# Optimization experiments

Hardware: AMD Instinct MI355X
Metric: run time of the kernel (lower is better)

## Reference

```python
import jax, jax.numpy as jnp
import numpy as np

B, N, C = 2, 2048, 768
H = 12
D = C // H
SCALE = D ** -0.5
EPS = 1e-5
HID = 4 * C


def layer_norm(x, g, b):
    mu = jnp.mean(x, axis=-1, keepdims=True)
    var = jnp.var(x, axis=-1, keepdims=True)
    return (x - mu) * jax.lax.rsqrt(var + EPS) * g + b


def setup_inputs():
    key = jax.random.key(0)
    ks = jax.random.split(key, 12)
    s = C ** -0.5
    x = jax.random.normal(ks[0], (B, N, C), dtype=jnp.float32)
    mask = (jax.random.uniform(ks[1], (B, N, N)) < 0.1).astype(jnp.float32)
    return {
        "x": x,
        "mask": mask,
        "g1": jnp.ones((C,), jnp.float32),
        "b1": jnp.zeros((C,), jnp.float32),
        "Wq": jax.random.normal(ks[2], (C, C), jnp.float32) * s,
        "Wkv": jax.random.normal(ks[3], (2 * C, C), jnp.float32) * s,
        "Wp": jax.random.normal(ks[4], (C, C), jnp.float32) * s,
        "bp": jnp.zeros((C,), jnp.float32),
        "g2": jnp.ones((C,), jnp.float32),
        "b2": jnp.zeros((C,), jnp.float32),
        "W1": jax.random.normal(ks[5], (HID, C), jnp.float32) * s,
        "bf1": jnp.zeros((HID,), jnp.float32),
        "W2": jax.random.normal(ks[6], (C, HID), jnp.float32) * (HID ** -0.5),
        "bf2": jnpmp if False else jnp.zeros((C,), jnp.float32),
    }


def block_fwd(x, mask, g1, b1, Wq, Wkv, Wp, bp, g2, b2, W1, bf1, W2, bf2):
    # --- attention branch (pre-norm) ---
    xn = layer_norm(x, g1, b1)
    q = (xn @ Wq.T).reshape(B, N, H, D).transpose(0, 2, 1, 3)      # bhnd
    kv = (xn @ Wkv.T).reshape(B, N, 2, H, D).transpose(2, 0, 3, 1, 4)
    k, v = kv[0], kv[1]                                             # bhnd
    attn = jnp.einsum('bhnd,bhmd->bhnm', q, k) * SCALE
    attn = attn + (mask * -100000.0)[:, None]                       # additive mask
    attn = jax.nn.softmax(attn, axis=-1)
    o = jnp.einsum('bhnm,bhmd->bhnd', attn, v)
    o = o.transpose(0, 2, 1, 3).reshape(B, N, C)
    o = o @ Wp.T + bp
    x = x + o
    # --- MLP branch (pre-norm) ---
    xn2 = layer_norm(x, g2, b2)
    h = jax.nn.gelu(xn2 @ W1.T + bf1, approximate=False)
    x = x + (h @ W2.T + bf2)
    return x


def reference(x, mask, g1, b1, Wq, Wkv, Wp, bp, g2, b2, W1, bf1, W2, bf2):
    return block_fwd(x, mask, g1, b1, Wq, Wkv, Wp, bp, g2, b2, W1, bf1, W2, bf2)
```

## Files before the change

kernel.cpp:

```cpp
#include <hip/hip_runtime.h>
#include <hip/hip_bf16.h>
#include <cstdint>
#include <cstddef>

#define BB 2
#define NN 2048
#define CC 768
#define HH 12
#define DD 64
#define HID 3072
#define TT (BB*NN)

typedef __attribute__((ext_vector_type(8))) short bf16x8;
typedef __attribute__((ext_vector_type(4))) short bf16x4;
typedef __attribute__((ext_vector_type(4))) float f32x4;
typedef __attribute__((ext_vector_type(4))) float float4v;
typedef __attribute__((ext_vector_type(4))) unsigned short ushort4v;
typedef __attribute__((ext_vector_type(8))) unsigned short ushort8v;

__device__ __forceinline__ unsigned short f2bf(float f) {
    unsigned int u = __float_as_uint(f);
    u += 0x7fffu + ((u >> 16) & 1u);
    return (unsigned short)(u >> 16);
}
__device__ __forceinline__ float bf2f(unsigned short u) {
    return __uint_as_float(((unsigned int)u) << 16);
}
#if __has_builtin(__builtin_amdgcn_exp2f)
#define EXP2F(x) __builtin_amdgcn_exp2f(x)
#else
#define EXP2F(x) exp2f(x)
#endif

__device__ __forceinline__ void gload16(const void* g, void* l) {
    __builtin_amdgcn_global_load_lds((__attribute__((address_space(1))) unsigned int*)g,
                                     (__attribute__((address_space(3))) unsigned int*)l,
                                     16, 0, 0);
}

#define WAITV(N) asm volatile("s_waitcnt vmcnt(" #N ")" ::: "memory")
#define WAITLGKM asm volatile("s_waitcnt lgkmcnt(0)" ::: "memory")

struct PrepArgs {
    const float* x; const float* g1; const float* b1; unsigned short* xn;
    const float* cin[5]; unsigned short* cout[5]; int n4[5];
    const float* mask; unsigned short* mb;
};
__global__ __launch_bounds__(256) void prep_kernel(PrepArgs a) {
    int id = blockIdx.x;
    int tid = threadIdx.x;
    if (id < TT) {
        const float* xr = a.x + (size_t)id * CC;
        float v0 = xr[tid], v1 = xr[tid + 256], v2 = xr[tid + 512];
        float s = v0 + v1 + v2;
        float s2 = v0 * v0 + v1 * v1 + v2 * v2;
#pragma unroll
        for (int off = 1; off < 64; off <<= 1) {
            s  += __shfl_xor(s, off);
            s2 += __shfl_xor(s2, off);
        }
        __shared__ float red[8];
        int wv = tid >> 6, lane = tid & 63;
        if (lane == 0) { red[wv] = s; red[wv + 4] = s2; }
        __syncthreads();
        s  = red[0] + red[1] + red[2] + red[3];
        s2 = red[4] + red[5] + red[6] + red[7];
        float mu   = s * (1.0f / CC);
        float var  = s2 * (1.0f / CC) - mu * mu;
        float rstd = rsqrtf(var + 1e-5f);
        unsigned short* orow = a.xn + (size_t)id * CC;
        orow[tid]       = f2bf((v0 - mu) * rstd * a.g1[tid]       + a.b1[tid]);
        orow[tid + 256] = f2bf((v1 - mu) * rstd * a.g1[tid + 256] + a.b1[tid + 256]);
        orow[tid + 512] = f2bf((v2 - mu) * rstd * a.g1[tid + 512] + a.b1[tid + 512]);
    } else if (id < TT + 1024) {
        int base = (id - TT) * 256 + tid;
        int stride = 1024 * 256;
#pragma unroll
        for (int sseg = 0; sseg < 5; ++sseg) {
            const float4v* ip = (const float4v*)a.cin[sseg];
            ushort4v* op = (ushort4v*)a.cout[sseg];
            for (int i = base; i < a.n4[sseg]; i += stride) {
                float4v v = ip[i];
                ushort4v o;
                o[0] = f2bf(v[0]); o[1] = f2bf(v[1]); o[2] = f2bf(v[2]); o[3] = f2bf(v[3]);
                op[i] = o;
            }
        }
    } else {
        int base = (id - TT - 1024) * 256 + tid;
        int stride = 1024 * 256;
        int n = BB * NN * (NN / 16);
        for (int i = base; i < n; i += stride) {
            const float4v* mp = (const float4v*)(a.mask + (size_t)i * 16);
            unsigned int bits = 0;
#pragma unroll
            for (int q = 0; q < 4; ++q) {
                float4v v = mp[q];
#pragma unroll
                for (int j = 0; j < 4; ++j) bits |= (v[j] > 0.5f) ? (1u << (q * 4 + j)) : 0u;
            }
            a.mb[i] = (unsigned short)bits;
        }
    }
}

__global__ __launch_bounds__(256) void ln_kernel(const float* __restrict__ x,
                                                 const float* __restrict__ g,
                                                 const float* __restrict__ b,
                                                 unsigned short* __restrict__ out) {
    int t = blockIdx.x;
    int tid = threadIdx.x;
    const float* xr = x + (size_t)t * CC;
    float v0 = xr[tid], v1 = xr[tid + 256], v2 = xr[tid + 512];
    float s = v0 + v1 + v2;
    float s2 = v0 * v0 + v1 * v1 + v2 * v2;
#pragma unroll
    for (int off = 1; off < 64; off <<= 1) {
        s  += __shfl_xor(s, off);
        s2 += __shfl_xor(s2, off);
    }
    __shared__ float red[8];
    int wv = tid >> 6, lane = tid & 63;
    if (lane == 0) { red[wv] = s; red[wv + 4] = s2; }
    __syncthreads();
    s  = red[0] + red[1] + red[2] + red[3];
    s2 = red[4] + red[5] + red[6] + red[7];
    float mu   = s * (1.0f / CC);
    float var  = s2 * (1.0f / CC) - mu * mu;
    float rstd = rsqrtf(var + 1e-5f);
    unsigned short* orow = out + (size_t)t * CC;
    orow[tid]       = f2bf((v0 - mu) * rstd * g[tid]       + b[tid]);
    orow[tid + 256] = f2bf((v1 - mu) * rstd * g[tid + 256] + b[tid + 256]);
    orow[tid + 512] = f2bf((v2 - mu) * rstd * g[tid + 512] + b[tid + 512]);
}

template <int EPI, int BM>
__global__ __launch_bounds__(256) void gemm_bt(const unsigned short* __restrict__ A,
                                               const unsigned short* __restrict__ Bw,
                                               const float* __restrict__ bias,
                                               const float* __restrict__ res,
                                               void* __restrict__ out,
                                               int M, int N, int K) {
    constexpr int MI = BM / 32;
    constexpr int NCA = (BM * 4) / 256;
    __shared__ alignas(16) unsigned short As[2][BM * 32];
    __shared__ alignas(16) unsigned short Bs[2][128 * 32];
    int tid = threadIdx.x;
    int lane = tid & 63, wv = tid >> 6;
    int l16 = lane & 15, lg = lane >> 4;
    int bm = blockIdx.x, bn = blockIdx.y;
    int wm = (wv & 1) * (BM / 2), wn = (wv >> 1) * 64;

    const unsigned short* Ab = A + (size_t)bm * BM * K;
    const unsigned short* Bb = Bw + (size_t)bn * 128 * K;

    const unsigned short* aSrc[NCA]; int aDst[NCA];
#pragma unroll
    for (int i = 0; i < NCA; ++i) {
        int c = tid + i * 256;
        int row = c >> 2, p = c & 3;
        int lc = p ^ ((row >> 1) & 3);
        aSrc[i] = Ab + (size_t)row * K + lc * 8;
        aDst[i] = c * 8;
    }
    const unsigned short* bSrc[2]; int bDst[2];
#pragma unroll
    for (int i = 0; i < 2; ++i) {
        int c = tid + i * 256;
        int row = c >> 2, p = c & 3;
        int lc = p ^ ((row >> 1) & 3);
        bSrc[i] = Bb + (size_t)row * K + lc * 8;
        bDst[i] = c * 8;
    }
    int aoff = (wm + l16) * 32 + ((lg ^ (((wm + l16) >> 1) & 3)) * 8);
    int boff = (wn + l16) * 32 + ((lg ^ (((wn + l16) >> 1) & 3)) * 8);

    f32x4 acc[MI][4];
#pragma unroll
    for (int i = 0; i < MI; ++i)
#pragma unroll
        for (int j = 0; j < 4; ++j) acc[i][j] = f32x4{0.f, 0.f, 0.f, 0.f};

    auto STAGE = [&](int s, int k0) {
#pragma unroll
        for (int i = 0; i < NCA; ++i) gload16(aSrc[i] + k0, &As[s][aDst[i]]);
#pragma unroll
        for (int i = 0; i < 2; ++i)   gload16(bSrc[i] + k0, &Bs[s][bDst[i]]);
    };

    STAGE(0, 0);
    int nt = K / 32;
    for (int t = 0; t < nt; ++t) {
        int cur = t & 1;
        if (t + 1 < nt) {
            STAGE(cur ^ 1, (t + 1) * 32);
            if constexpr (NCA + 2 == 4) { WAITV(4); } else { WAITV(3); }
        } else {
            WAITV(0);
        }
        __builtin_amdgcn_s_barrier();
        bf16x8 af[MI], bfr[4];
#pragma unroll
        for (int mi = 0; mi < MI; ++mi) af[mi]  = *(const bf16x8*)&As[cur][aoff + mi * 512];
#pragma unroll
        for (int ni = 0; ni < 4; ++ni)  bfr[ni] = *(const bf16x8*)&Bs[cur][boff + ni * 512];
#pragma unroll
        for (int mi = 0; mi < MI; ++mi)
#pragma unroll
            for (int ni = 0; ni < 4; ++ni)
                acc[mi][ni] = __builtin_amdgcn_mfma_f32_16x16x32_bf16(bfr[ni], af[mi], acc[mi][ni], 0, 0, 0);
        WAITLGKM;
        __builtin_amdgcn_s_barrier();
    }

#pragma unroll
    for (int mi = 0; mi < MI; ++mi) {
        int row = bm * BM + wm + mi * 16 + l16;
#pragma unroll
        for (int ni = 0; ni < 4; ++ni) {
            int col = bn * 128 + wn + ni * 16 + lg * 4;
            size_t idx = (size_t)row * N + col;
            f32x4 v = acc[mi][ni];
            if (EPI == 0) {
                bf16x4 ov;
#pragma unroll
                for (int r2 = 0; r2 < 4; ++r2) ov[r2] = (short)f2bf(v[r2]);
                *(bf16x4*)((unsigned short*)out + idx) = ov;
            } else if (EPI == 1 || EPI == 3) {
                f32x4 bv = *(const f32x4*)&bias[col];
                f32x4 rv = *(const f32x4*)&res[idx];
                f32x4 ov;
#pragma unroll
                for (int r2 = 0; r2 < 4; ++r2) ov[r2] = v[r2] + bv[r2] + rv[r2];
                *(f32x4*)((float*)out + idx) = ov;
            } else {
                f32x4 bv = *(const f32x4*)&bias[col];
                bf16x4 ov;
#pragma unroll
                for (int r2 = 0; r2 < 4; ++r2) {
                    float t2 = v[r2] + bv[r2];
                    t2 = 0.5f * t2 * (1.0f + erff(t2 * 0.70710678118f));
                    ov[r2] = (short)f2bf(t2);
                }
                *(bf16x4*)((unsigned short*)out + idx) = ov;
            }
        }
    }
}

#define KVB 64
#define HNT 16
#define VP 68
__global__ __launch_bounds__(256) void attn_kernel(const unsigned short* __restrict__ qkv,
                                                   const unsigned short* __restrict__ maskb,
                                                   float* __restrict__ Op,
                                                   float* __restrict__ lp) {
    __shared__ alignas(16) unsigned short Ks[2][64 * 64];
    __shared__ alignas(16) unsigned short Vt[2][64 * VP];
    int tid = threadIdx.x;
    int lane = tid & 63, wv = tid >> 6;
    int l16 = lane & 15, lg = lane >> 4;
    int id = blockIdx.x;
    int half = id & 1;
    int rid = id >> 1;
    int xcd = rid & 7, r = rid >> 3;
    int bh = xcd * 3 + (r % 3);
    int qb = r / 3;
    int b = bh / HH, h = bh % HH;
    int qrow = qb * 64 + wv * 16 + l16;
    int kt0 = half * HNT;

    const unsigned short* qp = qkv + ((size_t)(b * NN + qrow)) * 2304 + h * DD;
    bf16x8 q0r = *(const bf16x8*)(qp + 8 * lg);
    bf16x8 q1r = *(const bf16x8*)(qp + 32 + 8 * lg);
    const float QSC = 0.125f * 1.4426950408889634f;
    bf16x8 q0, q1;
#pragma unroll
    for (int j = 0; j < 8; ++j) {
        q0[j] = (short)f2bf(bf2f((unsigned short)q0r[j]) * QSC);
        q1[j] = (short)f2bf(bf2f((unsigned short)q1r[j]) * QSC);
    }

    const unsigned short* mrow  = maskb + ((size_t)(b * NN + qrow)) * 128;
    const unsigned short* kbase = qkv + (size_t)b * NN * 2304 + 768 + h * DD;
    const unsigned short* vbase = qkv + (size_t)b * NN * 2304 + 1536 + h * DD;

    const unsigned short* kSrc[2]; int kDst[2];
#pragma unroll
    for (int i = 0; i < 2; ++i) {
        int c = tid + i * 256;
        int row = c >> 3, p = c & 7;
        int lc = p ^ (row & 7);
        kSrc[i] = kbase + (size_t)row * 2304 + lc * 8;
        kDst[i] = c * 8;
    }
    int kp = tid & 31, dg = tid >> 5;
    const unsigned short* vSrc = vbase + (size_t)(2 * kp) * 2304 + dg * 8;

    int sw = l16 & 7;
    int kb0 = l16 * 64 + ((lg ^ sw) * 8);
    int kb1 = l16 * 64 + (((lg + 4) ^ sw) * 8);
    int vbo = l16 * VP + lg * 4;

    bf16x8 va, vb;
    unsigned long long mb_cur, mb_nxt;

    f32x4 oa[4];
#pragma unroll
    for (int i = 0; i < 4; ++i) oa[i] = f32x4{0.f, 0.f, 0.f, 0.f};
    float lrun = 0.f;

    auto LOAD = [&](int t, int s) {
        const unsigned short* vp = vSrc + (size_t)t * KVB * 2304;
        va = *(const bf16x8*)(vp);
        vb = *(const bf16x8*)(vp + 2304);
        mb_nxt = *(const unsigned long long*)(mrow + t * 4);
        __builtin_amdgcn_sched_barrier(0);
#pragma unroll
        for (int i = 0; i < 2; ++i) gload16(kSrc[i] + (size_t)t * KVB * 2304, &Ks[s][kDst[i]]);
    };
    auto WRITEV = [&](int s) {
        unsigned int* VtU = (unsigned int*)Vt[s];
#pragma unroll
        for (int j = 0; j < 8; ++j)
            VtU[(dg * 8 + j) * (VP / 2) + kp] =
                (unsigned int)(unsigned short)va[j] | ((unsigned int)(unsigned short)vb[j] << 16);
    };

    LOAD(kt0, 0);
    WAITV(2);
    WRITEV(0);
    mb_cur = mb_nxt;
    int cur = 0;

    for (int t = 0; t < HNT; ++t) {
        bool pre = (t + 1 < HNT);
        WAITV(0);
        WAITLGKM;
        __builtin_amdgcn_s_barrier();
        if (pre) LOAD(kt0 + t + 1, cur ^ 1);

        const unsigned short* Ksc = Ks[cur];
        const unsigned short* Vtc = Vt[cur];

        float ps = 0.f;
        bf16x4 pf[4];
#pragma unroll
        for (int ks = 0; ks < 4; ++ks) {
            bf16x8 k0 = *(const bf16x8*)&Ksc[kb0 + ks * 1024];
            bf16x8 k1 = *(const bf16x8*)&Ksc[kb1 + ks * 1024];
            f32x4 sa = f32x4{0.f, 0.f, 0.f, 0.f};
            sa = __builtin_amdgcn_mfma_f32_16x16x32_bf16(k0, q0, sa, 0, 0, 0);
            sa = __builtin_amdgcn_mfma_f32_16x16x32_bf16(k1, q1, sa, 0, 0, 0);
            unsigned int m16 = (unsigned int)(mb_cur >> (ks * 16 + lg * 4));
#pragma unroll
            for (int r2 = 0; r2 < 4; ++r2) {
                float mbit = (float)((m16 >> r2) & 1u);
                float p = EXP2F(fmaf(mbit, -144269.5f, sa[r2]));
                ps += p;
                pf[ks][r2] = (short)(__float_as_uint(p) >> 16);
            }
        }
        lrun += ps;

#pragma unroll
        for (int ks = 0; ks < 4; ++ks)
#pragma unroll
            for (int db = 0; db < 4; ++db) {
                bf16x4 vf = *(const bf16x4*)&Vtc[vbo + db * 16 * VP + ks * 16];
                oa[db] = __builtin_amdgcn_mfma_f32_16x16x16bf16_1k(vf, pf[ks], oa[db], 0, 0, 0);
            }

        if (pre) {
            WAITV(2);
            WRITEV(cur ^ 1);
            cur ^= 1;
            mb_cur = mb_nxt;
        }
    }

    float lt = lrun;
    lt += __shfl_xor(lt, 16);
    lt += __shfl_xor(lt, 32);
    lp[(size_t)half * TT * HH + (size_t)(b * NN + qrow) * HH + h] = lt;

    float* opf = Op + (size_t)half * TT * CC + (size_t)(b * NN + qrow) * CC + h * DD;
#pragma unroll
    for (int db = 0; db < 4; ++db)
        *(f32x4*)&opf[db * 16 + lg * 4] = oa[db];
}

__global__ __launch_bounds__(256) void combine_kernel(const float* __restrict__ Op,
                                                      const float* __restrict__ lp,
                                                      unsigned short* __restrict__ obuf) {
    int i8 = blockIdx.x * 256 + threadIdx.x;
    size_t i = (size_t)i8 * 8;
    int token = i8 / 96;
    int c8 = i8 % 96;
    int h = c8 >> 3;
    size_t lidx = (size_t)token * HH + h;
    float ls = lp[lidx] + lp[(size_t)TT * HH + lidx];
    float inv = 1.0f / ls;
    const float* O0 = Op;
    const float* O1 = Op + (size_t)TT * CC;
    f32x4 a0 = *(const f32x4*)&O0[i];
    f32x4 a1 = *(const f32x4*)&O0[i + 4];
    f32x4 b0 = *(const f32x4*)&O1[i];
    f32x4 b1 = *(const f32x4*)&O1[i + 4];
    ushort8v o;
#pragma unroll
    for (int j = 0; j < 4; ++j) o[j]     = f2bf((a0[j] + b0[j]) * inv);
#pragma unroll
    for (int j = 0; j < 4; ++j) o[4 + j] = f2bf((a1[j] + b1[j]) * inv);
    *(ushort8v*)&obuf[i] = o;
}

extern "C" void kernel_launch(void* const* d_in, const int* in_sizes, int n_in,
                              void* d_out, int out_size, void* d_ws, size_t ws_size,
                              hipStream_t stream) {
    const float* x    = (const float*)d_in[0];
    const float* mask = (const float*)d_in[1];
    const float* g1   = (const float*)d_in[2];
    const float* b1   = (const float*)d_in[3];
    const float* Wq   = (const float*)d_in[4];
    const float* Wkv  = (const float*)d_in[5];
    const float* Wp   = (const float*)d_in[6];
    const float* bp   = (const float*)d_in[7];
    const float* g2   = (const float*)d_in[8];
    const float* b2   = (const float*)d_in[9];
    const float* W1   = (const float*)d_in[10];
    const float* bf1  = (const float*)d_in[11];
    const float* W2   = (const float*)d_in[12];
    const float* bf2  = (const float*)d_in[13];
    float* out = (float*)d_out;

    char* w = (char*)d_ws;
    unsigned short* wqkv = (unsigned short*)w;      w += (size_t)2304 * 768 * 2;
    unsigned short* wp   = (unsigned short*)w;      w += (size_t)768 * 768 * 2;
    unsigned short* w1   = (unsigned short*)w;      w += (size_t)3072 * 768 * 2;
    unsigned short* w2   = (unsigned short*)w;      w += (size_t)768 * 3072 * 2;
    unsigned short* xn   = (unsigned short*)w;      w += (size_t)TT * CC * 2;
    unsigned short* qkv  = (unsigned short*)w;      w += (size_t)TT * 2304 * 2;
    unsigned short* mb   = (unsigned short*)w;      w += (size_t)BB * NN * 128 * 2;
    unsigned short* obuf = (unsigned short*)w;      w += (size_t)TT * CC * 2;
    float*          x1   = (float*)w;               w += (size_t)TT * CC * 4;
    unsigned short* xn2  = (unsigned short*)w;      w += (size_t)TT * CC * 2;
    unsigned short* hbuf = (unsigned short*)w;      w += (size_t)TT * HID * 2;

    float* Op = (float*)hbuf;
    float* lp = (float*)x1;

    PrepArgs pa;
    pa.x = x; pa.g1 = g1; pa.b1 = b1; pa.xn = xn;
    pa.cin[0] = Wq;  pa.cout[0] = wqkv;             pa.n4[0] = 768 * 768 / 4;
    pa.cin[1] = Wkv; pa.cout[1] = wqkv + 768 * 768; pa.n4[1] = 1536 * 768 / 4;
    pa.cin[2] = Wp;  pa.cout[2] = wp;               pa.n4[2] = 768 * 768 / 4;
    pa.cin[3] = W1;  pa.cout[3] = w1;               pa.n4[3] = 3072 * 768 / 4;
    pa.cin[4] = W2;  pa.cout[4] = w2;               pa.n4[4] = 768 * 3072 / 4;
    pa.mask = mask; pa.mb = mb;
    prep_kernel<<<TT + 2048, 256, 0, stream>>>(pa);

    gemm_bt<0, 128><<<dim3(TT / 128, 2304 / 128), 256, 0, stream>>>(xn, wqkv, nullptr, nullptr, qkv, TT, 2304, 768);

    attn_kernel<<<1536, 256, 0, stream>>>(qkv, mb, Op, lp);
    combine_kernel<<<TT * CC / 8 / 256, 256, 0, stream>>>(Op, lp, obuf);

    gemm_bt<1, 64><<<dim3(TT / 64, 768 / 128), 256, 0, stream>>>(obuf, wp, bp, x, x1, TT, 768, 768);

    ln_kernel<<<TT, 256, 0, stream>>>(x1, g2, b2, xn2);

    gemm_bt<2, 128><<<dim3(TT / 128, HID / 128), 256, 0, stream>>>(xn2, w1, bf1, nullptr, hbuf, TT, HID, 768);

    gemm_bt<3, 64><<<dim3(TT / 64, 768 / 128), 256, 0, stream>>>(hbuf, w2, bf2, x1, out, TT, 768, HID);
}
```

Measured before the change: 218.7 us.

## Use 256x256-tile 512-thread GEMM kernel for the MLP up-projection

Adds a new bf16 MFMA GEMM kernel with 256x256 output tiles, 8 waves, a double-buffered XOR-swizzled LDS layout and an fused bias+GELU epilogue. It is used for the W1 projection (4096x3072x768). Larger tiles raise arithmetic intensity and cut global reloads of A and B. In exchange the grid shrinks to 16x12=192 blocks, which may leave compute units underused, and the larger register and LDS footprint (128KB LDS) lowers occupancy.

```diff
diff --git a/kernel.cpp b/kernel.cpp
--- a/kernel.cpp
+++ b/kernel.cpp
@@ -233,6 +233,126 @@
 #pragma unroll
                 for (int r2 = 0; r2 < 4; ++r2) ov[r2] = v[r2] + bv[r2] + rv[r2];
                 *(f32x4*)((float*)out + idx) = ov;
+            } else {
+                f32x4 bv = *(const f32x4*)&bias[col];
+                bf16x4 ov;
+#pragma unroll
+                for (int r2 = 0; r2 < 4; ++r2) {
+                    float t2 = v[r2] + bv[r2];
+                    t2 = 0.5f * t2 * (1.0f + erff(t2 * 0.70710678118f));
+                    ov[r2] = (short)f2bf(t2);
+                }
+                *(bf16x4*)((unsigned short*)out + idx) = ov;
+            }
+        }
+    }
+}
+
+template <int EPI>
+__global__ __launch_bounds__(512) void gemm256(const unsigned short* __restrict__ A,
+                                               const unsigned short* __restrict__ Bw,
+                                               const float* __restrict__ bias,
+                                               const float* __restrict__ res,
+                                               void* __restrict__ out,
+                                               int M, int N, int K) {
+    __shared__ alignas(16) unsigned short As[2][256 * 64];
+    __shared__ alignas(16) unsigned short Bs[2][256 * 64];
+    int tid = threadIdx.x;
+    int lane = tid & 63, wv = tid >> 6;
+    int l16 = lane & 15, lg = lane >> 4;
+    int wr = wv >> 2, wc = wv & 3;
+    int bm = blockIdx.x, bn = blockIdx.y;
+
+    const unsigned short* Ab = A + (size_t)bm * 256 * K;
+    const unsigned short* Bb = Bw + (size_t)bn * 256 * K;
+
+    int off[4];
+#pragma unroll
+    for (int i = 0; i < 4; ++i) {
+        int c = tid + i * 512;
+        int row = c >> 3, p = c & 7;
+        int lc = p ^ (row & 7);
+        off[i] = row * K + lc * 8;
+    }
+
+    int arow = wr * 128 + l16;
+    int brow = wc * 64 + l16;
+    int s7 = l16 & 7;
+    int aoff0 = arow * 64 + ((lg ^ s7) * 8);
+    int aoff1 = arow * 64 + (((4 + lg) ^ s7) * 8);
+    int boff0 = brow * 64 + ((lg ^ s7) * 8);
+    int boff1 = brow * 64 + (((4 + lg) ^ s7) * 8);
+
+    f32x4 acc[8][4];
+#pragma unroll
+    for (int i = 0; i < 8; ++i)
+#pragma unroll
+        for (int j = 0; j < 4; ++j) acc[i][j] = f32x4{0.f, 0.f, 0.f, 0.f};
+
+    auto STAGE = [&](int s, int k0) {
+#pragma unroll
+        for (int i = 0; i < 4; ++i) {
+            gload16(Ab + off[i] + k0, (char*)As[s] + (size_t)tid * 16 + i * 8192);
+            gload16(Bb + off[i] + k0, (char*)Bs[s] + (size_t)tid * 16 + i * 8192);
+        }
+    };
+
+    STAGE(0, 0);
+    WAITV(0);
+    __builtin_amdgcn_s_barrier();
+    int nt = K / 64;
+    for (int t = 0; t < nt; ++t) {
+        int cur = t & 1;
+        if (t + 1 < nt) STAGE(cur ^ 1, (t + 1) * 64);
+
+        {
+            bf16x8 af[8], bfr[4];
+#pragma unroll
+            for (int mi = 0; mi < 8; ++mi) af[mi]  = *(const bf16x8*)&As[cur][aoff0 + mi * 1024];
+#pragma unroll
+            for (int ni = 0; ni < 4; ++ni) bfr[ni] = *(const bf16x8*)&Bs[cur][boff0 + ni * 1024];
+            WAITLGKM;
+            __builtin_amdgcn_s_setprio(1);
+#pragma unroll
+            for (int mi = 0; mi < 8; ++mi)
+#pragma unroll
+                for (int ni = 0; ni < 4; ++ni)
+                    acc[mi][ni] = __builtin_amdgcn_mfma_f32_16x16x32_bf16(bfr[ni], af[mi], acc[mi][ni], 0, 0, 0);
+            __builtin_amdgcn_s_setprio(0);
+        }
+        {
+            bf16x8 af[8], bfr[4];
+#pragma unroll
+            for (int mi = 0; mi < 8; ++mi) af[mi]  = *(const bf16x8*)&As[cur][aoff1 + mi * 1024];
+#pragma unroll
+            for (int ni = 0; ni < 4; ++ni) bfr[ni] = *(const bf16x8*)&Bs[cur][boff1 + ni * 1024];
+            WAITLGKM;
+            __builtin_amdgcn_s_setprio(1);
+#pragma unroll
+            for (int mi = 0; mi < 8; ++mi)
+#pragma unroll
+                for (int ni = 0; ni < 4; ++ni)
+                    acc[mi][ni] = __builtin_amdgcn_mfma_f32_16x16x32_bf16(bfr[ni], af[mi], acc[mi][ni], 0, 0, 0);
+            __builtin_amdgcn_s_setprio(0);
+        }
+
+        WAITV(0);
+        __builtin_amdgcn_s_barrier();
+    }
+
+#pragma unroll
+    for (int mi = 0; mi < 8; ++mi) {
+        int row = bm * 256 + wr * 128 + mi * 16 + l16;
+#pragma unroll
+        for (int ni = 0; ni < 4; ++ni) {
+            int col = bn * 256 + wc * 64 + ni * 16 + lg * 4;
+            size_t idx = (size_t)row * N + col;
+            f32x4 v = acc[mi][ni];
+            if (EPI == 0) {
+                bf16x4 ov;
+#pragma unroll
+                for (int r2 = 0; r2 < 4; ++r2) ov[r2] = (short)f2bf(v[r2]);
+                *(bf16x4*)((unsigned short*)out + idx) = ov;
             } else {
                 f32x4 bv = *(const f32x4*)&bias[col];
                 bf16x4 ov;
@@ -469,7 +589,7 @@
 
     ln_kernel<<<TT, 256, 0, stream>>>(x1, g2, b2, xn2);
 
-    gemm_bt<2, 128><<<dim3(TT / 128, HID / 128), 256, 0, stream>>>(xn2, w1, bf1, nullptr, hbuf, TT, HID, 768);
+    gemm256<2><<<dim3(TT / 256, HID / 256), 512, 0, stream>>>(xn2, w1, bf1, nullptr, hbuf, TT, HID, 768);
 
     gemm_bt<3, 64><<<dim3(TT / 64, 768 / 128), 256, 0, stream>>>(hbuf, w2, bf2, x1, out, TT, 768, HID);
 }
```

After: 245.6 us. +12.3%, slower.
